# Kernel optimization log

Measured on AMD Instinct MI355X. Metric: run time of the kernel, lower is better.

## Reference

```python
import jax, jax.numpy as jnp
import numpy as np

NUM_FRAMES = 6
HEADS = 16
DIM_HEAD = 64


def setup_inputs() -> dict:
    key = jax.random.key(0)
    ks = jax.random.split(key, 7)
    D = 1024
    x = jax.random.normal(ks[0], (12, 1024, D), dtype=jnp.float32)
    context = jax.random.normal(ks[1], (2, 1024, D), dtype=jnp.float32)
    s = 1.0 / np.sqrt(D)
    Wq = jax.random.normal(ks[2], (D, D), dtype=jnp.float32) * s
    Wk = jax.random.normal(ks[3], (D, D), dtype=jnp.float32) * s
    Wv = jax.random.normal(ks[4], (D, D), dtype=jnp.float32) * s
    Wo = jax.random.normal(ks[5], (D, D), dtype=jnp.float32) * s
    bo = jnp.zeros((D,), dtype=jnp.float32)
    return {"x": x, "context": context, "Wq": Wq, "Wk": Wk, "Wv": Wv, "Wo": Wo, "bo": bo}


def reference(x, context, Wq, Wk, Wv, Wo, bo):
    B, S, D = x.shape  # B=12, S=1024, D=1024
    scale = DIM_HEAD ** (-0.5)
    ab = B // NUM_FRAMES  # actual batch after frame inflation
    xr = x.reshape(ab, NUM_FRAMES * S, D)  # [ab, 6144, D]
    # Linear projections (torch Linear: y = x @ W.T)
    q = xr @ Wq.T            # [ab, Sq, inner]
    k = context @ Wk.T       # [ab, Sk, inner]
    v = context @ Wv.T
    Sq = q.shape[1]
    Sk = k.shape[1]
    q = q.reshape(ab, Sq, HEADS, DIM_HEAD).transpose(0, 2, 1, 3)  # [ab,h,Sq,d]
    k = k.reshape(ab, Sk, HEADS, DIM_HEAD).transpose(0, 2, 1, 3)
    v = v.reshape(ab, Sk, HEADS, DIM_HEAD).transpose(0, 2, 1, 3)
    attn = jnp.einsum("bhqd,bhkd->bhqk", q, k) * scale
    attn = jax.nn.softmax(attn, axis=-1)
    out = jnp.einsum("bhqk,bhkd->bhqd", attn, v)
    out = out.transpose(0, 2, 1, 3).reshape(ab, Sq, HEADS * DIM_HEAD)
    out = out @ Wo.T + bo  # dropout is identity at p=0 / eval
    return out.reshape(B, S, D)
```

## Files before the change

kernel.cpp:

```cpp
#include <hip/hip_runtime.h>

typedef short bf16x8 __attribute__((ext_vector_type(8)));
typedef float floatx4 __attribute__((ext_vector_type(4)));
typedef unsigned short u16;
typedef unsigned int u32;

__device__ __forceinline__ u16 f2bf(float f) {
  u32 u = __float_as_uint(f);
  u += 0x7FFF + ((u >> 16) & 1);
  return (u16)(u >> 16);
}
__device__ __forceinline__ u32 packbf(float a, float b) {
  return (u32)f2bf(a) | ((u32)f2bf(b) << 16);
}
__device__ __forceinline__ u32 permpack(u32 a_bits, u32 b_bits) {
  return __builtin_amdgcn_perm(b_bits, a_bits, 0x07060302u);
}

__device__ __forceinline__ float ex2(float x) {
#if __has_builtin(__builtin_amdgcn_exp2f)
  return __builtin_amdgcn_exp2f(x);
#else
  float r;
  asm("v_exp_f32 %0, %1" : "=v"(r) : "v"(x));
  return r;
#endif
}

__device__ __forceinline__ void gload_lds16(const u16* g, u16* l) {
  __builtin_amdgcn_global_load_lds(
      (const __attribute__((address_space(1))) void*)(const void*)g,
      (__attribute__((address_space(3))) void*)(void*)l, 16, 0, 0);
}

__device__ __forceinline__ int xcd_swz(int disp, int nwg) {
  const int q = nwg >> 3;
  return (disp & 7) * q + (disp >> 3);
}

__device__ __forceinline__ void bb_stage(const u16* Ag, const u16* Wg,
                                         u16* Asl, u16* Wsl) {
  gload_lds16(Ag, Asl);
  gload_lds16(Ag + 16 * 1024, Asl + 512);
  gload_lds16(Wg, Wsl);
  gload_lds16(Wg + 16 * 1024, Wsl + 512);
}

__device__ __forceinline__ void bb_frags(const u16* As, const u16* Ws, int wm,
                                         int wn, int m16, int quad,
                                         bf16x8 af[4], bf16x8 bfr[4]) {
#pragma unroll
  for (int t = 0; t < 4; ++t) {
    af[t]  = *(const bf16x8*)&As[(wm * 64 + t * 16 + m16) * 32 + quad * 8];
    bfr[t] = *(const bf16x8*)&Ws[(wn * 64 + t * 16 + m16) * 32 + quad * 8];
  }
}

__device__ __forceinline__ void bb_mfma(const bf16x8 af[4], const bf16x8 bfr[4],
                                        floatx4 acc[4][4]) {
#pragma unroll
  for (int i = 0; i < 4; ++i)
#pragma unroll
    for (int j = 0; j < 4; ++j)
      acc[i][j] = __builtin_amdgcn_mfma_f32_16x16x32_bf16(af[i], bfr[j],
                                                          acc[i][j], 0, 0, 0);
}

__device__ __forceinline__ void bb_mainloop(const u16* __restrict__ A,
                                            const u16* __restrict__ W,
                                            u16* As0, u16* Ws0, u16* As1,
                                            u16* Ws1, int m0, int n0,
                                            floatx4 acc[4][4]) {
  const int tid = threadIdx.x, lane = tid & 63, w = tid >> 6;
  const int wm = w & 1, wn = w >> 1;
  const int m16 = lane & 15, quad = lane >> 4;
  const int lr = lane >> 2;
  const int sc = (lane & 3) * 8;

  const u16* Ag = A + (size_t)(m0 + w * 32 + lr) * 1024 + sc;
  const u16* Wg = W + (size_t)(n0 + w * 32 + lr) * 1024 + sc;
  const int so = (w * 32) * 32;

#pragma unroll
  for (int i = 0; i < 4; ++i)
#pragma unroll
    for (int j = 0; j < 4; ++j) acc[i][j] = (floatx4)0.0f;

  bb_stage(Ag, Wg, As0 + so, Ws0 + so);
  __syncthreads();

  bf16x8 af[4], bfr[4];
  for (int kt = 0; kt < 32; kt += 2) {
    bb_frags(As0, Ws0, wm, wn, m16, quad, af, bfr);
    __builtin_amdgcn_sched_barrier(0);
    bb_stage(Ag + (kt + 1) * 32, Wg + (kt + 1) * 32, As1 + so, Ws1 + so);
    __builtin_amdgcn_sched_barrier(0);
    bb_mfma(af, bfr, acc);
    __syncthreads();
    bb_frags(As1, Ws1, wm, wn, m16, quad, af, bfr);
    __builtin_amdgcn_sched_barrier(0);
    if (kt + 2 < 32)
      bb_stage(Ag + (kt + 2) * 32, Wg + (kt + 2) * 32, As0 + so, Ws0 + so);
    __builtin_amdgcn_sched_barrier(0);
    bb_mfma(af, bfr, acc);
    __syncthreads();
  }
}

__global__ __launch_bounds__(256) void gemm_qkv(
    const u16* __restrict__ xb, const u16* __restrict__ ctxb,
    const u16* __restrict__ wqb, const u16* __restrict__ wkb,
    const u16* __restrict__ wvb, u16* __restrict__ Qb, u16* __restrict__ Kbuf,
    u16* __restrict__ Vtb) {
  __shared__ u16 As0[128 * 32];
  __shared__ u16 Ws0[128 * 32];
  __shared__ u16 As1[128 * 32];
  __shared__ u16 Ws1[128 * 32];
  const int lane = threadIdx.x & 63, w = threadIdx.x >> 6;
  const int wm = w & 1, wn = w >> 1;
  const int m16 = lane & 15, quad = lane >> 4;
  const int disp = blockIdx.y * 8 + blockIdx.x;
  const int work = xcd_swz(disp, 1024);
  const int y = work >> 3;
  const int n0 = (work & 7) * 128;
  const u16 *A, *W;
  int m0, mode;
  if (y < 96)       { A = xb;   W = wqb; m0 = y * 128;         mode = 0; }
  else if (y < 112) { A = ctxb; W = wkb; m0 = (y - 96) * 128;  mode = 1; }
  else              { A = ctxb; W = wvb; m0 = (y - 112) * 128; mode = 2; }
  floatx4 acc[4][4];
  bb_mainloop(A, W, As0, Ws0, As1, Ws1, m0, n0, acc);
  const float cs = (mode == 0) ? 0.18033688011112042f : 1.0f;
#pragma unroll
  for (int j = 0; j < 4; ++j) {
    const int col = n0 + wn * 64 + j * 16 + m16;
#pragma unroll
    for (int i = 0; i < 4; ++i)
#pragma unroll
      for (int r = 0; r < 4; ++r) {
        const int row = m0 + wm * 64 + i * 16 + quad * 4 + r;
        const u16 v = f2bf(acc[i][j][r] * cs);
        if (mode == 0)
          Qb[(size_t)row * 1024 + col] = v;
        else if (mode == 1)
          Kbuf[(size_t)row * 1024 + col] = v;
        else
          Vtb[((size_t)((row >> 10) * 1024 + col)) * 1024 + (row & 1023)] = v;
      }
  }
}

__global__ __launch_bounds__(256) void gemm_out(const u16* __restrict__ A,
                                                const u16* __restrict__ W,
                                                float* __restrict__ C,
                                                const float* __restrict__ bias) {
  __shared__ u16 As0[128 * 32];
  __shared__ u16 Ws0[128 * 32];
  __shared__ u16 As1[128 * 32];
  __shared__ u16 Ws1[128 * 32];
  const int lane = threadIdx.x & 63, w = threadIdx.x >> 6;
  const int wm = w & 1, wn = w >> 1;
  const int m16 = lane & 15, quad = lane >> 4;
  const int disp = blockIdx.y * 8 + blockIdx.x;
  const int work = xcd_swz(disp, 768);
  const int n0 = (work & 7) * 128, m0 = (work >> 3) * 128;
  floatx4 acc[4][4];
  bb_mainloop(A, W, As0, Ws0, As1, Ws1, m0, n0, acc);
#pragma unroll
  for (int j = 0; j < 4; ++j) {
    const int col = n0 + wn * 64 + j * 16 + m16;
    const float bv = bias[col];
#pragma unroll
    for (int i = 0; i < 4; ++i)
#pragma unroll
      for (int r = 0; r < 4; ++r) {
        const int row = m0 + wm * 64 + i * 16 + quad * 4 + r;
        C[(size_t)row * 1024 + col] = acc[i][j][r] + bv;
      }
  }
}

__global__ __launch_bounds__(256) void cvt_all(
    const float* __restrict__ x, const float* __restrict__ ctx,
    const float* __restrict__ wq, const float* __restrict__ wk,
    const float* __restrict__ wv, const float* __restrict__ wo,
    u16* __restrict__ xb, u16* __restrict__ ctxb, u16* __restrict__ wqb,
    u16* __restrict__ wkb, u16* __restrict__ wvb, u16* __restrict__ wob) {
  const u32 i = blockIdx.x * 256 + threadIdx.x;
  const float* s;
  u16* d;
  u32 o;
  if (i < 3145728u)      { s = x;   d = xb;   o = i; }
  else if (i < 3670016u) { s = ctx; d = ctxb; o = i - 3145728u; }
  else if (i < 3932160u) { s = wq;  d = wqb;  o = i - 3670016u; }
  else if (i < 4194304u) { s = wk;  d = wkb;  o = i - 3932160u; }
  else if (i < 4456448u) { s = wv;  d = wvb;  o = i - 4194304u; }
  else                   { s = wo;  d = wob;  o = i - 4456448u; }
  const float4 v = ((const float4*)s)[o];
  uint2 p;
  p.x = packbf(v.x, v.y);
  p.y = packbf(v.z, v.w);
  ((uint2*)d)[o] = p;
}

__global__ __launch_bounds__(256, 4) void attn_flash(
    const u16* __restrict__ Q, const u16* __restrict__ Kb,
    const u16* __restrict__ Vt, u16* __restrict__ O) {
  __shared__ u16 Kl[2 * 64 * 32];
  __shared__ u16 Vl[2 * 64 * 32];
  __shared__ u32 Pl[4 * 32 * 36];
  const int tid = threadIdx.x, lane = tid & 63, w = tid >> 6;
  const int m16 = lane & 15, quad = lane >> 4;
  const int disp =
      blockIdx.x + 48 * (blockIdx.y + 16 * blockIdx.z);
  const int work = xcd_swz(disp, 1536);
  const int qx = work % 48;
  const int bh = work / 48;
  const int h = bh & 15, b = bh >> 4;
  const int q0 = qx * 128 + w * 32;
  u32* const pbase = &Pl[w * 32 * 36];

  bf16x8 aq[2][2];
#pragma unroll
  for (int qt = 0; qt < 2; ++qt)
#pragma unroll
    for (int ks = 0; ks < 2; ++ks)
      aq[qt][ks] =
          *(const bf16x8*)&Q[((size_t)(b * 6144 + q0 + qt * 16 + m16)) * 1024 +
                             h * 64 + ks * 32 + quad * 8];

  const int wk = w & 1, wh = w >> 1;
  const u16* kg = Kb + ((size_t)(b * 1024 + wh * 32 + (lane >> 2))) * 1024 +
                  h * 64 + wk * 32 + (lane & 3) * 8;
  const u16* vg = Vt + ((size_t)(b * 16 + h)) * 65536 +
                  (size_t)(wh * 32 + (lane >> 2)) * 1024 + wk * 32 +
                  (lane & 3) * 8;
  u16* const klb = &Kl[wk * 2048 + wh * 1024];
  u16* const vlb = &Vl[wk * 2048 + wh * 1024];

  bf16x8 vone;
#pragma unroll
  for (int e = 0; e < 8; ++e) vone[e] = (short)0x3F80;

  floatx4 oacc[2][4];
#pragma unroll
  for (int qt = 0; qt < 2; ++qt)
#pragma unroll
    for (int mtd = 0; mtd < 4; ++mtd) oacc[qt][mtd] = (floatx4)0.0f;
  floatx4 lacc[2];
  lacc[0] = (floatx4)0.0f;
  lacc[1] = (floatx4)0.0f;

#pragma unroll 1
  for (int kt = 0; kt < 16; ++kt) {
    gload_lds16(kg, klb);
    gload_lds16(kg + 16 * 1024, klb + 512);
    gload_lds16(vg, vlb);
    gload_lds16(vg + 16 * 1024, vlb + 512);
    kg += 64 * 1024;
    vg += 64;
    __syncthreads();

    floatx4 sst[2][4];
#pragma unroll
    for (int mt = 0; mt < 4; ++mt) {
      const int row = mt * 16 + m16;
      const bf16x8 kf0 = *(const bf16x8*)&Kl[row * 32 + quad * 8];
      const bf16x8 kf1 = *(const bf16x8*)&Kl[2048 + row * 32 + quad * 8];
#pragma unroll
      for (int qt = 0; qt < 2; ++qt) {
        floatx4 t = (floatx4)0.0f;
        t = __builtin_amdgcn_mfma_f32_16x16x32_bf16(kf0, aq[qt][0], t, 0, 0, 0);
        sst[qt][mt] =
            __builtin_amdgcn_mfma_f32_16x16x32_bf16(kf1, aq[qt][1], t, 0, 0, 0);
      }
    }
#pragma unroll
    for (int qt = 0; qt < 2; ++qt) {
      u32* const prow = &pbase[(qt * 16 + m16) * 36 + quad * 2];
#pragma unroll
      for (int mt = 0; mt < 4; ++mt) {
        const u32 b0 = __float_as_uint(ex2(sst[qt][mt][0]));
        const u32 b1 = __float_as_uint(ex2(sst[qt][mt][1]));
        const u32 b2 = __float_as_uint(ex2(sst[qt][mt][2]));
        const u32 b3 = __float_as_uint(ex2(sst[qt][mt][3]));
        uint2 pk;
        pk.x = permpack(b0, b1);
        pk.y = permpack(b2, b3);
        *(uint2*)&prow[mt * 8] = pk;
      }
    }
#pragma unroll
    for (int kk = 0; kk < 2; ++kk) {
      bf16x8 pf[2];
#pragma unroll
      for (int qt = 0; qt < 2; ++qt)
        pf[qt] =
            *(const bf16x8*)&pbase[(qt * 16 + m16) * 36 + kk * 16 + quad * 4];
      lacc[0] = __builtin_amdgcn_mfma_f32_16x16x32_bf16(vone, pf[0], lacc[0],
                                                        0, 0, 0);
      lacc[1] = __builtin_amdgcn_mfma_f32_16x16x32_bf16(vone, pf[1], lacc[1],
                                                        0, 0, 0);
#pragma unroll
      for (int mtd = 0; mtd < 4; ++mtd) {
        const bf16x8 vf =
            *(const bf16x8*)&Vl[kk * 2048 + (mtd * 16 + m16) * 32 + quad * 8];
#pragma unroll
        for (int qt = 0; qt < 2; ++qt)
          oacc[qt][mtd] = __builtin_amdgcn_mfma_f32_16x16x32_bf16(
              vf, pf[qt], oacc[qt][mtd], 0, 0, 0);
      }
    }
    __syncthreads();
  }

#pragma unroll
  for (int qt = 0; qt < 2; ++qt) {
    const float linv = 1.0f / lacc[qt][0];
    const size_t obase =
        ((size_t)(b * 6144 + q0 + qt * 16 + m16)) * 1024 + h * 64;
#pragma unroll
    for (int mtd = 0; mtd < 4; ++mtd) {
      const int d0 = mtd * 16 + quad * 4;
      *(u32*)&O[obase + d0] =
          packbf(oacc[qt][mtd][0] * linv, oacc[qt][mtd][1] * linv);
      *(u32*)&O[obase + d0 + 2] =
          packbf(oacc[qt][mtd][2] * linv, oacc[qt][mtd][3] * linv);
    }
  }
}

template <bool A_BF16, bool OUT_F32, int VT, bool BIAS>
__global__ __launch_bounds__(256) void gemm_nt(
    const void* __restrict__ Ap, const float* __restrict__ W,
    void* __restrict__ Cp, const float* __restrict__ bias, int M, int N,
    int K, float scale) {
  __shared__ u16 As[128 * 40];
  __shared__ u16 Ws[128 * 40];
  const int tid = threadIdx.x;
  const int lane = tid & 63;
  const int wv = tid >> 6;
  const int wm = wv & 1, wn = wv >> 1;
  const int m16 = lane & 15, quad = lane >> 4;
  const int n0 = blockIdx.x * 128;
  const int m0 = blockIdx.y * 128;
  const int lr = tid >> 2;
  const int lc = (tid & 3) * 8;
  floatx4 acc[4][4];
#pragma unroll
  for (int i = 0; i < 4; ++i)
#pragma unroll
    for (int j = 0; j < 4; ++j) acc[i][j] = (floatx4)0.0f;
  const int KT = K >> 5;
  for (int kt = 0; kt < KT; ++kt) {
    const int k0 = kt << 5;
#pragma unroll
    for (int j = 0; j < 2; ++j) {
      const int r = lr + 64 * j;
      if (A_BF16) {
        *(uint4*)&As[r * 40 + lc] =
            *(const uint4*)&((const u16*)Ap)[(size_t)(m0 + r) * K + k0 + lc];
      } else {
        const float* Arow = (const float*)Ap + (size_t)(m0 + r) * K + k0 + lc;
        const float4 a0 = *(const float4*)Arow;
        const float4 a1 = *(const float4*)(Arow + 4);
        uint4 p;
        p.x = packbf(a0.x, a0.y); p.y = packbf(a0.z, a0.w);
        p.z = packbf(a1.x, a1.y); p.w = packbf(a1.z, a1.w);
        *(uint4*)&As[r * 40 + lc] = p;
      }
      const float* Wrow = W + (size_t)(n0 + r) * K + k0 + lc;
      const float4 w0 = *(const float4*)Wrow;
      const float4 w1 = *(const float4*)(Wrow + 4);
      uint4 q;
      q.x = packbf(w0.x, w0.y); q.y = packbf(w0.z, w0.w);
      q.z = packbf(w1.x, w1.y); q.w = packbf(w1.z, w1.w);
      *(uint4*)&Ws[r * 40 + lc] = q;
    }
    __syncthreads();
    bf16x8 af[4], bfr[4];
#pragma unroll
    for (int t = 0; t < 4; ++t) {
      af[t]  = *(const bf16x8*)&As[(wm * 64 + t * 16 + m16) * 40 + quad * 8];
      bfr[t] = *(const bf16x8*)&Ws[(wn * 64 + t * 16 + m16) * 40 + quad * 8];
    }
#pragma unroll
    for (int i = 0; i < 4; ++i)
#pragma unroll
      for (int j = 0; j < 4; ++j)
        acc[i][j] = __builtin_amdgcn_mfma_f32_16x16x32_bf16(af[i], bfr[j],
                                                            acc[i][j], 0, 0, 0);
    __syncthreads();
  }
#pragma unroll
  for (int j = 0; j < 4; ++j) {
    const int col = n0 + wn * 64 + j * 16 + m16;
    const float bv = BIAS ? bias[col] : 0.0f;
#pragma unroll
    for (int i = 0; i < 4; ++i)
#pragma unroll
      for (int r = 0; r < 4; ++r) {
        const int row = m0 + wm * 64 + i * 16 + quad * 4 + r;
        const float v = acc[i][j][r] * scale + bv;
        if (OUT_F32)
          ((float*)Cp)[(size_t)row * N + col] = v;
        else if (VT)
          ((u16*)Cp)[((size_t)((row >> 10) * 1024 + col)) * 1024 +
                     (row & 1023)] = f2bf(v);
        else
          ((u16*)Cp)[(size_t)row * N + col] = f2bf(v);
      }
  }
}

extern "C" void kernel_launch(void* const* d_in, const int* in_sizes, int n_in,
                              void* d_out, int out_size, void* d_ws,
                              size_t ws_size, hipStream_t stream) {
  const float* x   = (const float*)d_in[0];
  const float* ctx = (const float*)d_in[1];
  const float* Wq  = (const float*)d_in[2];
  const float* Wk  = (const float*)d_in[3];
  const float* Wv  = (const float*)d_in[4];
  const float* Wo  = (const float*)d_in[5];
  const float* bo  = (const float*)d_in[6];
  float* out = (float*)d_out;
  const dim3 blk(256);
  const float CS = 0.18033688011112042f;

  u16* Qb   = (u16*)d_ws;
  u16* Kbuf = Qb + 12582912;
  u16* Vtb  = Kbuf + 2097152;
  u16* Obx  = Vtb + 2097152;
  u16* ctxb = Obx + 12582912;
  u16* wqb  = ctxb + 2097152;
  u16* wkb  = wqb + 1048576;
  u16* wvb  = wkb + 1048576;
  u16* wob  = wvb + 1048576;
  const size_t need = (size_t)(wob + 1048576 - Qb) * sizeof(u16);

  if (ws_size >= need) {
    cvt_all<<<18432, blk, 0, stream>>>(x, ctx, Wq, Wk, Wv, Wo, Obx, ctxb, wqb,
                                       wkb, wvb, wob);
    gemm_qkv<<<dim3(8, 128), blk, 0, stream>>>(Obx, ctxb, wqb, wkb, wvb, Qb,
                                               Kbuf, Vtb);
    attn_flash<<<dim3(48, 16, 2), blk, 0, stream>>>(Qb, Kbuf, Vtb, Obx);
    gemm_out<<<dim3(8, 96), blk, 0, stream>>>(Obx, wob, out, bo);
  } else {
    gemm_nt<false, false, 0, false><<<dim3(8, 96), blk, 0, stream>>>(
        x, Wq, Qb, nullptr, 12288, 1024, 1024, CS);
    gemm_nt<false, false, 0, false><<<dim3(8, 16), blk, 0, stream>>>(
        ctx, Wk, Kbuf, nullptr, 2048, 1024, 1024, 1.0f);
    gemm_nt<false, false, 1, false><<<dim3(8, 16), blk, 0, stream>>>(
        ctx, Wv, Vtb, nullptr, 2048, 1024, 1024, 1.0f);
    attn_flash<<<dim3(48, 16, 2), blk, 0, stream>>>(Qb, Kbuf, Vtb, Obx);
    gemm_nt<true, true, 0, true><<<dim3(8, 96), blk, 0, stream>>>(
        Obx, Wo, out, bo, 12288, 1024, 1024, 1.0f);
  }
}
```

Measured before the change: 299.2 us.

## Reorder QKV GEMM pipeline with manual waitcnt barriers; single-buffer output GEMM

The QKV projection GEMM mainloop now issues the next tile's global-to-LDS staging before reading fragments. It replaces __syncthreads and sched_barriers with an explicit vmcnt(0) wait plus s_barrier, so the compiler can interleave loads and MFMAs freely. The output GEMM reverts to a simple single-buffered loop with two syncs per k-step and half the shared memory, trading load/compute overlap for possibly higher occupancy. The manual waitcnt relies on bb_stage's stores to LDS being complete once vmcnt drains; whether that holds depends on how bb_stage is written.

```diff
diff --git a/kernel.cpp b/kernel.cpp
--- a/kernel.cpp
+++ b/kernel.cpp
@@ -68,8 +68,7 @@
 
 __device__ __forceinline__ void bb_mainloop(const u16* __restrict__ A,
                                             const u16* __restrict__ W,
-                                            u16* As0, u16* Ws0, u16* As1,
-                                            u16* Ws1, int m0, int n0,
+                                            u16* As, u16* Ws, int m0, int n0,
                                             floatx4 acc[4][4]) {
   const int tid = threadIdx.x, lane = tid & 63, w = tid >> 6;
   const int wm = w & 1, wn = w >> 1;
@@ -79,6 +78,39 @@
 
   const u16* Ag = A + (size_t)(m0 + w * 32 + lr) * 1024 + sc;
   const u16* Wg = W + (size_t)(n0 + w * 32 + lr) * 1024 + sc;
+  u16* const Asl = &As[(w * 32) * 32];
+  u16* const Wsl = &Ws[(w * 32) * 32];
+
+#pragma unroll
+  for (int i = 0; i < 4; ++i)
+#pragma unroll
+    for (int j = 0; j < 4; ++j) acc[i][j] = (floatx4)0.0f;
+
+  for (int kt = 0; kt < 32; ++kt) {
+    bb_stage(Ag, Wg, Asl, Wsl);
+    Ag += 32;
+    Wg += 32;
+    __syncthreads();
+    bf16x8 af[4], bfr[4];
+    bb_frags(As, Ws, wm, wn, m16, quad, af, bfr);
+    bb_mfma(af, bfr, acc);
+    __syncthreads();
+  }
+}
+
+__device__ __forceinline__ void bb_mainloop_pipe(const u16* __restrict__ A,
+                                                 const u16* __restrict__ W,
+                                                 u16* As0, u16* Ws0, u16* As1,
+                                                 u16* Ws1, int m0, int n0,
+                                                 floatx4 acc[4][4]) {
+  const int tid = threadIdx.x, lane = tid & 63, w = tid >> 6;
+  const int wm = w & 1, wn = w >> 1;
+  const int m16 = lane & 15, quad = lane >> 4;
+  const int lr = lane >> 2;
+  const int sc = (lane & 3) * 8;
+
+  const u16* Ag = A + (size_t)(m0 + w * 32 + lr) * 1024 + sc;
+  const u16* Wg = W + (size_t)(n0 + w * 32 + lr) * 1024 + sc;
   const int so = (w * 32) * 32;
 
 #pragma unroll
@@ -87,23 +119,22 @@
     for (int j = 0; j < 4; ++j) acc[i][j] = (floatx4)0.0f;
 
   bb_stage(Ag, Wg, As0 + so, Ws0 + so);
-  __syncthreads();
+  asm volatile("s_waitcnt vmcnt(0)" ::: "memory");
+  __builtin_amdgcn_s_barrier();
 
   bf16x8 af[4], bfr[4];
   for (int kt = 0; kt < 32; kt += 2) {
+    bb_stage(Ag + (kt + 1) * 32, Wg + (kt + 1) * 32, As1 + so, Ws1 + so);
     bb_frags(As0, Ws0, wm, wn, m16, quad, af, bfr);
-    __builtin_amdgcn_sched_barrier(0);
-    bb_stage(Ag + (kt + 1) * 32, Wg + (kt + 1) * 32, As1 + so, Ws1 + so);
-    __builtin_amdgcn_sched_barrier(0);
     bb_mfma(af, bfr, acc);
-    __syncthreads();
-    bb_frags(As1, Ws1, wm, wn, m16, quad, af, bfr);
-    __builtin_amdgcn_sched_barrier(0);
+    asm volatile("s_waitcnt vmcnt(0)" ::: "memory");
+    __builtin_amdgcn_s_barrier();
     if (kt + 2 < 32)
       bb_stage(Ag + (kt + 2) * 32, Wg + (kt + 2) * 32, As0 + so, Ws0 + so);
-    __builtin_amdgcn_sched_barrier(0);
+    bb_frags(As1, Ws1, wm, wn, m16, quad, af, bfr);
     bb_mfma(af, bfr, acc);
-    __syncthreads();
+    asm volatile("s_waitcnt vmcnt(0)" ::: "memory");
+    __builtin_amdgcn_s_barrier();
   }
 }
 
@@ -129,7 +160,7 @@
   else if (y < 112) { A = ctxb; W = wkb; m0 = (y - 96) * 128;  mode = 1; }
   else              { A = ctxb; W = wvb; m0 = (y - 112) * 128; mode = 2; }
   floatx4 acc[4][4];
-  bb_mainloop(A, W, As0, Ws0, As1, Ws1, m0, n0, acc);
+  bb_mainloop_pipe(A, W, As0, Ws0, As1, Ws1, m0, n0, acc);
   const float cs = (mode == 0) ? 0.18033688011112042f : 1.0f;
 #pragma unroll
   for (int j = 0; j < 4; ++j) {
@@ -154,10 +185,8 @@
                                                 const u16* __restrict__ W,
                                                 float* __restrict__ C,
                                                 const float* __restrict__ bias) {
-  __shared__ u16 As0[128 * 32];
-  __shared__ u16 Ws0[128 * 32];
-  __shared__ u16 As1[128 * 32];
-  __shared__ u16 Ws1[128 * 32];
+  __shared__ u16 As[128 * 32];
+  __shared__ u16 Ws[128 * 32];
   const int lane = threadIdx.x & 63, w = threadIdx.x >> 6;
   const int wm = w & 1, wn = w >> 1;
   const int m16 = lane & 15, quad = lane >> 4;
@@ -165,7 +194,7 @@
   const int work = xcd_swz(disp, 768);
   const int n0 = (work & 7) * 128, m0 = (work >> 3) * 128;
   floatx4 acc[4][4];
-  bb_mainloop(A, W, As0, Ws0, As1, Ws1, m0, n0, acc);
+  bb_mainloop(A, W, As, Ws, m0, n0, acc);
 #pragma unroll
   for (int j = 0; j < 4; ++j) {
     const int col = n0 + wn * 64 + j * 16 + m16;
```

New measurement: 288.6 us. -3.5%, faster.
